# Kernel tuning notes

Hardware: AMD Instinct MI355X
Metric: run time of the kernel (lower is better)

Reference implementation:

```python
import jax, jax.numpy as jnp
import numpy as np

N = 50000
D = 64
E = 800000


def setup_inputs() -> dict:
    key = jax.random.key(0)
    ks = jax.random.split(key, 8)
    x = jax.random.normal(ks[0], (N, D), dtype=jnp.float32)
    edge_index = jax.random.randint(ks[1], (2, E), 0, N, dtype=jnp.int64)
    edge_attr = jax.random.normal(ks[2], (E,), dtype=jnp.float32)
    x_agg_emb = jax.random.normal(ks[3], (N, D), dtype=jnp.float32)
    # Linear(2D -> D) weights stored as [in, out]; scale ~ kaiming-ish
    W_msg = jax.random.normal(ks[4], (2 * D, D), dtype=jnp.float32) * (1.0 / np.sqrt(2 * D))
    b_msg = jnp.zeros((D,), dtype=jnp.float32)
    W_upd = jax.random.normal(ks[5], (2 * D, D), dtype=jnp.float32) * (1.0 / np.sqrt(2 * D))
    b_upd = jnp.zeros((D,), dtype=jnp.float32)
    return {"x": x, "edge_index": edge_index, "edge_attr": edge_attr,
            "x_agg_emb": x_agg_emb, "W_msg": W_msg, "b_msg": b_msg,
            "W_upd": W_upd, "b_upd": b_upd}


def reference(x, edge_index, edge_attr, x_agg_emb, W_msg, b_msg, W_upd, b_upd):
    col, row = edge_index[0], edge_index[1]
    # edge-weighted gather: [E, D]
    msgs = edge_attr[:, None] * x[col]
    # scatter-mean over destination nodes (dim_size = N)
    summed = jax.ops.segment_sum(msgs, row, num_segments=N)            # [N, D]
    counts = jax.ops.segment_sum(jnp.ones_like(edge_attr), row, num_segments=N)  # [N]
    x_agg = summed / jnp.maximum(counts, 1.0)[:, None]
    # message MLP: Linear(2D->D) + ReLU
    m = jax.nn.relu(jnp.concatenate([x_agg, x_agg_emb], axis=-1) @ W_msg + b_msg)
    # update MLP: Linear(2D->D) + ReLU
    out = jax.nn.relu(jnp.concatenate([x, m], axis=-1) @ W_upd + b_upd)
    return out
```

## Files before the change

### kernel.cpp

```cpp
#include <hip/hip_runtime.h>


#define CAP 48
#define FILLB 2048
#define CVTB 1024

typedef __attribute__((ext_vector_type(8))) short short8;
typedef __attribute__((ext_vector_type(4))) float f32x4;

__device__ __forceinline__ unsigned short f2bf(float f) {
    unsigned int u = __float_as_uint(f);
    u += 0x7FFFu + ((u >> 16) & 1u);
    return (unsigned short)(u >> 16);
}
__device__ __forceinline__ float bf2f(unsigned short h) {
    return __uint_as_float((unsigned)h << 16);
}
__device__ __forceinline__ uint4 pack8(const float* v) {
    uint4 r;
    r.x = (unsigned)f2bf(v[0]) | ((unsigned)f2bf(v[1]) << 16);
    r.y = (unsigned)f2bf(v[2]) | ((unsigned)f2bf(v[3]) << 16);
    r.z = (unsigned)f2bf(v[4]) | ((unsigned)f2bf(v[5]) << 16);
    r.w = (unsigned)f2bf(v[6]) | ((unsigned)f2bf(v[7]) << 16);
    return r;
}

__global__ __launch_bounds__(256) void zero_f32(float* p, int n) {
    int i = blockIdx.x * 256 + threadIdx.x;
    if (i < n) p[i] = 0.0f;
}
__global__ __launch_bounds__(256) void zero_i32(int* p, int n) {
    int i = blockIdx.x * 256 + threadIdx.x;
    if (i < n) p[i] = 0;
}

__global__ __launch_bounds__(256) void cvt_zero_group(
    const float* __restrict__ x, unsigned short* __restrict__ xh,
    int* __restrict__ cnt, uint4* __restrict__ pk4, int N)
{
    const int g    = blockIdx.x & 7;
    const int bg   = blockIdx.x >> 3;
    const int nb   = gridDim.x >> 3;
    const int rpg  = (N + 7) >> 3;
    const int rlo  = g * rpg;
    const int rhi  = min(rlo + rpg, N);
    const int nrows = rhi - rlo;
    const int tid  = bg * 256 + (int)threadIdx.x;
    const int nthr = nb * 256;

    for (int c = tid; c < nrows * 8; c += nthr) {
        size_t base = ((size_t)rlo * 8 + c) * 8;
        const float* src = x + base;
        float4 p0 = ((const float4*)src)[0];
        float4 p1 = ((const float4*)src)[1];
        float v[8];
        v[0] = p0.x; v[1] = p0.y; v[2] = p0.z; v[3] = p0.w;
        v[4] = p1.x; v[5] = p1.y; v[6] = p1.z; v[7] = p1.w;
        *(uint4*)&xh[base] = pack8(v);
    }
    for (int c = tid; c < nrows; c += nthr) cnt[rlo + c] = 0;
    const uint4 z = make_uint4(0u, 0u, 0u, 0u);
    const size_t pbase = (size_t)rlo * (CAP / 2);
    for (size_t c = tid; c < (size_t)nrows * (CAP / 2); c += nthr)
        pk4[pbase + c] = z;
}

__global__ __launch_bounds__(256) void fill_group_kernel(
    const int* __restrict__ ei, const float* __restrict__ ea,
    int* cnt, int2* __restrict__ packed, int E, int N)
{
    const int g   = blockIdx.x & 7;
    const int bg  = blockIdx.x >> 3;
    const int nb  = gridDim.x >> 3;
    const int rpg = (N + 7) >> 3;
    const int rlo = g * rpg;
    const int rhi = min(rlo + rpg, N);
    const int chunk = (E + nb - 1) / nb;
    const int lo = bg * chunk;
    const int hi = min(lo + chunk, E);
    int e = lo + (int)threadIdx.x;
    for (; e + 768 < hi; e += 1024) {
        int r0 = ei[E + e];
        int r1 = ei[E + e + 256];
        int r2 = ei[E + e + 512];
        int r3 = ei[E + e + 768];
        int c0 = ei[e], c1 = ei[e + 256], c2 = ei[e + 512], c3 = ei[e + 768];
        float a0 = ea[e], a1 = ea[e + 256], a2 = ea[e + 512], a3 = ea[e + 768];
        bool m0 = (r0 >= rlo) & (r0 < rhi);
        bool m1 = (r1 >= rlo) & (r1 < rhi);
        bool m2 = (r2 >= rlo) & (r2 < rhi);
        bool m3 = (r3 >= rlo) & (r3 < rhi);
        int p0 = CAP, p1 = CAP, p2 = CAP, p3 = CAP;
        if (m0) p0 = atomicAdd(&cnt[r0], 1);
        if (m1) p1 = atomicAdd(&cnt[r1], 1);
        if (m2) p2 = atomicAdd(&cnt[r2], 1);
        if (m3) p3 = atomicAdd(&cnt[r3], 1);
        if (m0 && p0 < CAP) packed[(size_t)r0 * CAP + p0] = make_int2(c0, __float_as_int(a0));
        if (m1 && p1 < CAP) packed[(size_t)r1 * CAP + p1] = make_int2(c1, __float_as_int(a1));
        if (m2 && p2 < CAP) packed[(size_t)r2 * CAP + p2] = make_int2(c2, __float_as_int(a2));
        if (m3 && p3 < CAP) packed[(size_t)r3 * CAP + p3] = make_int2(c3, __float_as_int(a3));
    }
    for (; e < hi; e += 256) {
        int row = ei[E + e];
        if (row >= rlo && row < rhi) {
            int pos = atomicAdd(&cnt[row], 1);
            if (pos < CAP)
                packed[(size_t)row * CAP + pos] = make_int2(ei[e], __float_as_int(ea[e]));
        }
    }
}


__device__ __forceinline__ void stage_W512(
    unsigned short* Wb, const float* Wg, int t)
{
    #pragma unroll
    for (int c = t; c < 1024; c += 512) {
        int R = c >> 6, nn = c & 63;
        int kt = R >> 2, qq = R & 3;
        const float* src = Wg + (size_t)(kt * 32 + qq * 8) * 64 + nn;
        float v[8];
        #pragma unroll
        for (int j = 0; j < 8; j++) v[j] = src[(size_t)j * 64];
        *(uint4*)&Wb[R * 528 + nn * 8] = pack8(v);
    }
}

#define CONSUME(D)                                                          \
    {                                                                       \
        unsigned short u0[8], u1[8];                                        \
        _Pragma("unroll")                                                   \
        for (int n = 0; n < 8; n++) {                                       \
            unsigned v0 = ((unsigned)D[n].x << 7) + lane2;                  \
            unsigned v1 = ((unsigned)D[n].z << 7) + lane2;                  \
            u0[n] = *(const unsigned short*)((const char*)xh + v0);         \
            u1[n] = *(const unsigned short*)((const char*)xh + v1);         \
        }                                                                   \
        _Pragma("unroll")                                                   \
        for (int n = 0; n < 8; n++) {                                       \
            ac0[n] += __int_as_float(D[n].y) * bf2f(u0[n]);                 \
            ac1[n] += __int_as_float(D[n].w) * bf2f(u1[n]);                 \
        }                                                                   \
    }

__global__ __launch_bounds__(512) void gather_mlp(
    const int2* __restrict__ packed, const int* __restrict__ cnt,
    const unsigned short* __restrict__ xh, const float* __restrict__ emb,
    const float* __restrict__ Wm, const float* __restrict__ bm,
    const float* __restrict__ Wu, const float* __restrict__ bu,
    float* __restrict__ out, int N)
{
    __shared__ __align__(16) unsigned short Ab [64 * 128];
    __shared__ __align__(16) unsigned short Ab2[64 * 128];
    __shared__ __align__(16) unsigned short Wb [16 * 528];
    __shared__ __align__(16) unsigned short Wb2[16 * 528];

    const int t    = threadIdx.x;
    const int g    = blockIdx.x & 7;
    const int tile = blockIdx.x >> 3;
    const int rpg  = (N + 7) >> 3;
    const int rlo  = g * rpg;
    const int rhi  = min(rlo + rpg, N);
    const int tile0 = rlo + tile * 64;
    const int lane = t & 63;
    const int q = lane >> 4, ln = lane & 15;
    const unsigned lane2 = (unsigned)lane * 2;
    const int wu = __builtin_amdgcn_readfirstlane(t >> 6);

    stage_W512(Wb,  Wm, t);
    stage_W512(Wb2, Wu, t);
    {
        int r = t >> 3, c = t & 7;
        int node = tile0 + r;
        uint4 d = make_uint4(0u, 0u, 0u, 0u);
        if (node < rhi)
            d = *(const uint4*)&xh[(size_t)node * 64 + c * 8];
        *(uint4*)&Ab2[r * 128 + ((c ^ (r & 15)) * 8)] = d;
    }
    {
        int r = t >> 3, c = t & 7;
        int node = tile0 + r;
        float v[8] = {0.f, 0.f, 0.f, 0.f, 0.f, 0.f, 0.f, 0.f};
        if (node < rhi) {
            const float* src = emb + (size_t)node * 64 + c * 8;
            float4 p0 = ((const float4*)src)[0];
            float4 p1 = ((const float4*)src)[1];
            v[0] = p0.x; v[1] = p0.y; v[2] = p0.z; v[3] = p0.w;
            v[4] = p1.x; v[5] = p1.y; v[6] = p1.z; v[7] = p1.w;
        }
        int ch = 8 + c;
        *(uint4*)&Ab[r * 128 + ((ch ^ (r & 15)) * 8)] = pack8(v);
    }

    const int4* s4 = (const int4*)packed;
    int seg[8], deg[8];
    int maxdl = 0;
    #pragma unroll
    for (int n = 0; n < 8; n++) {
        int node = tile0 + wu * 8 + n;
        bool ok = node < rhi;
        int nd = ok ? node : rlo;
        seg[n] = nd * (CAP / 2);
        deg[n] = ok ? cnt[node] : 0;
        maxdl  = max(maxdl, ok ? min(deg[n], CAP) : 0);
    }
    float ac0[8], ac1[8];
    #pragma unroll
    for (int n = 0; n < 8; n++) { ac0[n] = 0.f; ac1[n] = 0.f; }

    int maxb = (maxdl + 1) >> 1;
    int4 dc[8], dn[8];
    #pragma unroll
    for (int n = 0; n < 8; n++) dc[n] = s4[seg[n]];
    int jb = 0;
    while (jb < maxb) {
        int jn = min(jb + 1, CAP / 2 - 1);
        #pragma unroll
        for (int n = 0; n < 8; n++) dn[n] = s4[seg[n] + jn];
        CONSUME(dc);
        jb++;
        if (jb >= maxb) break;
        int jn2 = min(jb + 1, CAP / 2 - 1);
        #pragma unroll
        for (int n = 0; n < 8; n++) dc[n] = s4[seg[n] + jn2];
        CONSUME(dn);
        jb++;
    }

    #pragma unroll
    for (int n = 0; n < 8; n++) {
        int r = wu * 8 + n;
        int node = tile0 + r;
        float mean = (node < rhi)
            ? (ac0[n] + ac1[n]) / fmaxf((float)deg[n], 1.0f) : 0.f;
        int ch = lane >> 3;
        Ab[r * 128 + ((ch ^ (r & 15)) * 8) + (lane & 7)] = f2bf(mean);
    }
    __syncthreads();

    const int wr = wu & 3;
    const int wn0 = (wu >> 2) * 2, wn1 = wn0 + 1;
    f32x4 acc0 = (f32x4){0.f, 0.f, 0.f, 0.f};
    f32x4 acc1 = (f32x4){0.f, 0.f, 0.f, 0.f};
    {
        const int rr = wr * 16 + ln;
        #pragma unroll
        for (int kt = 0; kt < 4; kt++) {
            short8 af = *(const short8*)&Ab[rr * 128 + (((kt * 4 + q) ^ ln) * 8)];
            short8 bf0 = *(const short8*)&Wb[(kt * 4 + q) * 528 + (wn0 * 16 + ln) * 8];
            short8 bf1 = *(const short8*)&Wb[(kt * 4 + q) * 528 + (wn1 * 16 + ln) * 8];
            acc0 = __builtin_amdgcn_mfma_f32_16x16x32_bf16(af, bf0, acc0, 0, 0, 0);
            acc1 = __builtin_amdgcn_mfma_f32_16x16x32_bf16(af, bf1, acc1, 0, 0, 0);
        }
    }

    {
        float bmv0 = bm[wn0 * 16 + ln];
        float bmv1 = bm[wn1 * 16 + ln];
        #pragma unroll
        for (int reg = 0; reg < 4; reg++) {
            int rr = wr * 16 + q * 4 + reg;
            {
                float mv = fmaxf(acc0[reg] + bmv0, 0.f);
                int k  = 64 + wn0 * 16 + ln;
                int ch = k >> 3;
                Ab2[rr * 128 + ((ch ^ (rr & 15)) * 8) + (k & 7)] = f2bf(mv);
            }
            {
                float mv = fmaxf(acc1[reg] + bmv1, 0.f);
                int k  = 64 + wn1 * 16 + ln;
                int ch = k >> 3;
                Ab2[rr * 128 + ((ch ^ (rr & 15)) * 8) + (k & 7)] = f2bf(mv);
            }
        }
    }
    __syncthreads();

    f32x4 acc2a = (f32x4){0.f, 0.f, 0.f, 0.f};
    f32x4 acc2b = (f32x4){0.f, 0.f, 0.f, 0.f};
    {
        const int rr = wr * 16 + ln;
        #pragma unroll
        for (int kt = 0; kt < 4; kt++) {
            short8 af = *(const short8*)&Ab2[rr * 128 + (((kt * 4 + q) ^ ln) * 8)];
            short8 bf0 = *(const short8*)&Wb2[(kt * 4 + q) * 528 + (wn0 * 16 + ln) * 8];
            short8 bf1 = *(const short8*)&Wb2[(kt * 4 + q) * 528 + (wn1 * 16 + ln) * 8];
            acc2a = __builtin_amdgcn_mfma_f32_16x16x32_bf16(af, bf0, acc2a, 0, 0, 0);
            acc2b = __builtin_amdgcn_mfma_f32_16x16x32_bf16(af, bf1, acc2b, 0, 0, 0);
        }
    }
    {
        float buv0 = bu[wn0 * 16 + ln];
        float buv1 = bu[wn1 * 16 + ln];
        #pragma unroll
        for (int reg = 0; reg < 4; reg++) {
            int rr = wr * 16 + q * 4 + reg;
            int node = tile0 + rr;
            if (node < rhi) {
                out[(size_t)node * 64 + wn0 * 16 + ln] = fmaxf(acc2a[reg] + buv0, 0.f);
                out[(size_t)node * 64 + wn1 * 16 + ln] = fmaxf(acc2b[reg] + buv1, 0.f);
            }
        }
    }
}


__global__ __launch_bounds__(256) void hist_kernel(
    const int* __restrict__ ei, int* hist, int E)
{
    int e = blockIdx.x * 256 + threadIdx.x;
    if (e < E) atomicAdd(&hist[ei[E + e]], 1);
}
__global__ __launch_bounds__(256) void scan_partial_kernel(
    const int* __restrict__ hist, int* partial, int N)
{
    __shared__ int s[256];
    int t = threadIdx.x;
    int i = blockIdx.x * 256 + t;
    s[t] = (i < N) ? hist[i] : 0;
    __syncthreads();
    #pragma unroll
    for (int off = 128; off > 0; off >>= 1) {
        if (t < off) s[t] += s[t + off];
        __syncthreads();
    }
    if (t == 0) partial[blockIdx.x] = s[0];
}
__global__ __launch_bounds__(256) void scan_top_kernel(
    const int* __restrict__ partial, int* scanP, int NB)
{
    __shared__ int s[256];
    int t = threadIdx.x;
    int v = (t < NB) ? partial[t] : 0;
    s[t] = v;
    __syncthreads();
    #pragma unroll
    for (int off = 1; off < 256; off <<= 1) {
        int add = (t >= off) ? s[t - off] : 0;
        __syncthreads();
        s[t] += add;
        __syncthreads();
    }
    if (t < NB) scanP[t] = s[t] - v;
}
__global__ __launch_bounds__(256) void scan_final_kernel(
    const int* __restrict__ hist, const int* __restrict__ scanP,
    int* offsets, int* cursor, int N)
{
    __shared__ int s[256];
    int t = threadIdx.x;
    int i = blockIdx.x * 256 + t;
    int v = (i < N) ? hist[i] : 0;
    s[t] = v;
    __syncthreads();
    #pragma unroll
    for (int off = 1; off < 256; off <<= 1) {
        int add = (t >= off) ? s[t - off] : 0;
        __syncthreads();
        s[t] += add;
        __syncthreads();
    }
    if (i < N) {
        int o = scanP[blockIdx.x] + s[t] - v;
        offsets[i] = o;
        cursor[i]  = o;
    }
}
__global__ __launch_bounds__(256) void fill_kernel(
    const int* __restrict__ ei, const float* __restrict__ ea,
    int* cursor, int2* __restrict__ packed, int E)
{
    int e = blockIdx.x * 256 + threadIdx.x;
    if (e >= E) return;
    int pos = atomicAdd(&cursor[ei[E + e]], 1);
    packed[pos] = make_int2(ei[e], __float_as_int(ea[e]));
}
__global__ __launch_bounds__(256) void gather_kernel(
    const int2* __restrict__ packed, const int* __restrict__ offsets,
    const int* __restrict__ hist, const float* __restrict__ x,
    float* __restrict__ out, int N)
{
    int t = threadIdx.x;
    int n = blockIdx.x * 4 + (t >> 6);
    int lane = t & 63;
    if (n >= N) return;
    int start = offsets[n];
    int deg   = hist[n];
    float a0 = 0.f, a1 = 0.f, a2 = 0.f, a3 = 0.f;
    int j = 0;
    for (; j + 4 <= deg; j += 4) {
        int2 p0 = packed[start + j];
        int2 p1 = packed[start + j + 1];
        int2 p2 = packed[start + j + 2];
        int2 p3 = packed[start + j + 3];
        a0 += __int_as_float(p0.y) * x[(size_t)p0.x * 64 + lane];
        a1 += __int_as_float(p1.y) * x[(size_t)p1.x * 64 + lane];
        a2 += __int_as_float(p2.y) * x[(size_t)p2.x * 64 + lane];
        a3 += __int_as_float(p3.y) * x[(size_t)p3.x * 64 + lane];
    }
    for (; j < deg; j++) {
        int2 p = packed[start + j];
        a0 += __int_as_float(p.y) * x[(size_t)p.x * 64 + lane];
    }
    float acc = (a0 + a1) + (a2 + a3);
    out[(size_t)n * 64 + lane] = acc / fmaxf((float)deg, 1.0f);
}


__global__ __launch_bounds__(256) void scatter_kernel(
    const int* __restrict__ ei, const float* __restrict__ ea,
    const float* __restrict__ x, float* summed, float* counts, int E)
{
    int idx = blockIdx.x * 256 + threadIdx.x;
    int e = idx >> 6;
    int d = idx & 63;
    if (e >= E) return;
    float v = ea[e] * x[(size_t)ei[e] * 64 + d];
    atomicAdd(&summed[(size_t)ei[E + e] * 64 + d], v);
    if (d == 0) atomicAdd(&counts[ei[E + e]], 1.0f);
}


__device__ __forceinline__ void stage_W(
    unsigned short* Wb, const float* Wg, int t)
{
    #pragma unroll
    for (int c = t; c < 1024; c += 256) {
        int R = c >> 6, nn = c & 63;
        int kt = R >> 2, qq = R & 3;
        const float* src = Wg + (size_t)(kt * 32 + qq * 8) * 64 + nn;
        float v[8];
        #pragma unroll
        for (int j = 0; j < 8; j++) v[j] = src[(size_t)j * 64];
        *(uint4*)&Wb[R * 528 + nn * 8] = pack8(v);
    }
}

__device__ __forceinline__ void mfma_tile(
    const unsigned short* Ab, const unsigned short* Wb,
    int wv, int lane, f32x4 acc[4])
{
    const int q  = lane >> 4;
    const int ln = lane & 15;
    const int rr = wv * 16 + ln;
    short8 af[4];
    #pragma unroll
    for (int kt = 0; kt < 4; kt++)
        af[kt] = *(const short8*)&Ab[rr * 128 + (((kt * 4 + q) ^ ln) * 8)];
    #pragma unroll
    for (int nt = 0; nt < 4; nt++) {
        #pragma unroll
        for (int kt = 0; kt < 4; kt++) {
            short8 bf = *(const short8*)&Wb[(kt * 4 + q) * 528 + (nt * 16 + ln) * 8];
            acc[nt] = __builtin_amdgcn_mfma_f32_16x16x32_bf16(af[kt], bf, acc[nt], 0, 0, 0);
        }
    }
}

__global__ __launch_bounds__(256) void mfma_mlp(
    const float* Aagg, const float* __restrict__ Aemb,
    const float* __restrict__ counts, const float* __restrict__ Xin,
    const float* __restrict__ Wm, const float* __restrict__ bm,
    const float* __restrict__ Wu, const float* __restrict__ bu,
    float* out, int N)
{
    __shared__ __align__(16) unsigned short Ab[64 * 128];
    __shared__ __align__(16) unsigned short Wb[16 * 528];

    const int t = threadIdx.x;
    const int tile0 = blockIdx.x * 64;
    const int lane = t & 63, wv = t >> 6;
    const int q = lane >> 4, ln = lane & 15;

    stage_W(Wb, Wm, t);
    #pragma unroll
    for (int s = t; s < 1024; s += 256) {
        int r = s >> 4, chunk = s & 15;
        int node = tile0 + r;
        float v[8] = {0.f, 0.f, 0.f, 0.f, 0.f, 0.f, 0.f, 0.f};
        if (node < N) {
            const float* src = (chunk < 8)
                ? (Aagg + (size_t)node * 64 + chunk * 8)
                : (Aemb + (size_t)node * 64 + (chunk - 8) * 8);
            float4 p0 = ((const float4*)src)[0];
            float4 p1 = ((const float4*)src)[1];
            v[0] = p0.x; v[1] = p0.y; v[2] = p0.z; v[3] = p0.w;
            v[4] = p1.x; v[5] = p1.y; v[6] = p1.z; v[7] = p1.w;
            if (counts && chunk < 8) {
                float rc = 1.0f / fmaxf(counts[node], 1.0f);
                #pragma unroll
                for (int i = 0; i < 8; i++) v[i] *= rc;
            }
        }
        *(uint4*)&Ab[r * 128 + ((chunk ^ (r & 15)) * 8)] = pack8(v);
    }
    __syncthreads();

    f32x4 acc[4];
    #pragma unroll
    for (int nt = 0; nt < 4; nt++) acc[nt] = (f32x4){0.f, 0.f, 0.f, 0.f};
    mfma_tile(Ab, Wb, wv, lane, acc);
    __syncthreads();

    stage_W(Wb, Wu, t);
    #pragma unroll
    for (int s = t; s < 512; s += 256) {
        int r = s >> 3, chunk = s & 7;
        int node = tile0 + r;
        float v[8] = {0.f, 0.f, 0.f, 0.f, 0.f, 0.f, 0.f, 0.f};
        if (node < N) {
            const float* src = Xin + (size_t)node * 64 + chunk * 8;
            float4 p0 = ((const float4*)src)[0];
            float4 p1 = ((const float4*)src)[1];
            v[0] = p0.x; v[1] = p0.y; v[2] = p0.z; v[3] = p0.w;
            v[4] = p1.x; v[5] = p1.y; v[6] = p1.z; v[7] = p1.w;
        }
        *(uint4*)&Ab[r * 128 + ((chunk ^ (r & 15)) * 8)] = pack8(v);
    }
    #pragma unroll
    for (int nt = 0; nt < 4; nt++) {
        float bmv = bm[nt * 16 + ln];
        #pragma unroll
        for (int reg = 0; reg < 4; reg++) {
            float mv = fmaxf(acc[nt][reg] + bmv, 0.f);
            int rr = wv * 16 + q * 4 + reg;
            int k  = 64 + nt * 16 + ln;
            int ch = k >> 3;
            Ab[rr * 128 + ((ch ^ (rr & 15)) * 8) + (k & 7)] = f2bf(mv);
        }
    }
    __syncthreads();

    f32x4 acc2[4];
    #pragma unroll
    for (int nt = 0; nt < 4; nt++) acc2[nt] = (f32x4){0.f, 0.f, 0.f, 0.f};
    mfma_tile(Ab, Wb, wv, lane, acc2);
    #pragma unroll
    for (int nt = 0; nt < 4; nt++) {
        float buv = bu[nt * 16 + ln];
        #pragma unroll
        for (int reg = 0; reg < 4; reg++) {
            int rr = wv * 16 + q * 4 + reg;
            int node = tile0 + rr;
            if (node < N)
                out[(size_t)node * 64 + nt * 16 + ln] =
                    fmaxf(acc2[nt][reg] + buv, 0.f);
        }
    }
}

extern "C" void kernel_launch(void* const* d_in, const int* in_sizes, int n_in,
                              void* d_out, int out_size, void* d_ws, size_t ws_size,
                              hipStream_t stream) {
    const float* x   = (const float*)d_in[0];
    const int*   ei  = (const int*)d_in[1];
    const float* ea  = (const float*)d_in[2];
    const float* emb = (const float*)d_in[3];
    const float* Wm  = (const float*)d_in[4];
    const float* bm  = (const float*)d_in[5];
    const float* Wu  = (const float*)d_in[6];
    const float* bu  = (const float*)d_in[7];
    float*       out = (float*)d_out;

    const int N = in_sizes[0] / 64;
    const int E = in_sizes[2];
    const int NB = (N + 255) / 256;

    const int eblocks = (E + 255) / 256;
    const int mblocks = (N + 63) / 64;
    const int rpg = (N + 7) / 8;

    const size_t need_cap = (size_t)N * CAP * 8 + (size_t)N * 128 + (size_t)N * 4;
    const size_t need_csr = (size_t)E * 8 + ((size_t)3 * N + 512) * 4;

    if (ws_size >= need_cap) {
        char* ws = (char*)d_ws;
        int2*           packed = (int2*)ws;
        unsigned short* xh     = (unsigned short*)(ws + (size_t)N * CAP * 8);
        int*            cnt    = (int*)(ws + (size_t)N * CAP * 8 + (size_t)N * 128);

        cvt_zero_group<<<CVTB, 256, 0, stream>>>(x, xh, cnt, (uint4*)packed, N);
        fill_group_kernel<<<FILLB, 256, 0, stream>>>(ei, ea, cnt, packed, E, N);
        int tpg = (rpg + 63) / 64;
        gather_mlp<<<8 * tpg, 512, 0, stream>>>(packed, cnt, xh, emb,
                                                Wm, bm, Wu, bu, out, N);
    } else if (ws_size >= need_csr && NB <= 256) {
        char* ws = (char*)d_ws;
        int2* packed  = (int2*)ws;
        int*  hist    = (int*)(ws + (size_t)E * 8);
        int*  offsets = hist + N;
        int*  cursor  = offsets + N;
        int*  partial = cursor + N;
        int*  scanP   = partial + 256;

        zero_i32<<<NB, 256, 0, stream>>>(hist, N);
        hist_kernel<<<eblocks, 256, 0, stream>>>(ei, hist, E);
        scan_partial_kernel<<<NB, 256, 0, stream>>>(hist, partial, N);
        scan_top_kernel<<<1, 256, 0, stream>>>(partial, scanP, NB);
        scan_final_kernel<<<NB, 256, 0, stream>>>(hist, scanP, offsets, cursor, N);
        fill_kernel<<<eblocks, 256, 0, stream>>>(ei, ea, cursor, packed, E);
        gather_kernel<<<(N + 3) / 4, 256, 0, stream>>>(packed, offsets, hist, x, out, N);
        mfma_mlp<<<mblocks, 256, 0, stream>>>(out, emb, nullptr, x,
                                              Wm, bm, Wu, bu, out, N);
    } else {
        float* counts = (float*)d_ws;
        zero_f32<<<(N * 64 + 255) / 256, 256, 0, stream>>>(out, N * 64);
        zero_f32<<<NB, 256, 0, stream>>>(counts, N);
        long long total = (long long)E * 64;
        scatter_kernel<<<(int)((total + 255) / 256), 256, 0, stream>>>(
            ei, ea, x, out, counts, E);
        mfma_mlp<<<mblocks, 256, 0, stream>>>(out, emb, counts, x,
                                              Wm, bm, Wu, bu, out, N);
    }
}
```

Before: 163.5 us.

## Reuse one LDS activation buffer and simplify gather loop for higher occupancy

Drops the second 16 KB activation buffer by holding the x tile in registers and writing it into the same buffer after the first MLP, with an extra barrier. The gather loop loses its explicit double-buffered prefetch of edge records and now loads per-iteration in two groups of four nodes. Degree is made wave-uniform and a min-waves launch bound is added. Together these cut LDS and register use to fit more blocks per CU, at the cost of less explicit memory-latency hiding within each wave.

```diff
diff --git a/kernel.cpp b/kernel.cpp
--- a/kernel.cpp
+++ b/kernel.cpp
@@ -126,24 +126,7 @@
     }
 }
 
-#define CONSUME(D)                                                          \
-    {                                                                       \
-        unsigned short u0[8], u1[8];                                        \
-        _Pragma("unroll")                                                   \
-        for (int n = 0; n < 8; n++) {                                       \
-            unsigned v0 = ((unsigned)D[n].x << 7) + lane2;                  \
-            unsigned v1 = ((unsigned)D[n].z << 7) + lane2;                  \
-            u0[n] = *(const unsigned short*)((const char*)xh + v0);         \
-            u1[n] = *(const unsigned short*)((const char*)xh + v1);         \
-        }                                                                   \
-        _Pragma("unroll")                                                   \
-        for (int n = 0; n < 8; n++) {                                       \
-            ac0[n] += __int_as_float(D[n].y) * bf2f(u0[n]);                 \
-            ac1[n] += __int_as_float(D[n].w) * bf2f(u1[n]);                 \
-        }                                                                   \
-    }
-
-__global__ __launch_bounds__(512) void gather_mlp(
+__global__ __launch_bounds__(512, 6) void gather_mlp(
     const int2* __restrict__ packed, const int* __restrict__ cnt,
     const unsigned short* __restrict__ xh, const float* __restrict__ emb,
     const float* __restrict__ Wm, const float* __restrict__ bm,
@@ -151,7 +134,6 @@
     float* __restrict__ out, int N)
 {
     __shared__ __align__(16) unsigned short Ab [64 * 128];
-    __shared__ __align__(16) unsigned short Ab2[64 * 128];
     __shared__ __align__(16) unsigned short Wb [16 * 528];
     __shared__ __align__(16) unsigned short Wb2[16 * 528];
 
@@ -169,62 +151,80 @@
 
     stage_W512(Wb,  Wm, t);
     stage_W512(Wb2, Wu, t);
+    const int sr = t >> 3, sc = t & 7;
+    uint4 xreg = make_uint4(0u, 0u, 0u, 0u);
+    if (tile0 + sr < rhi)
+        xreg = *(const uint4*)&xh[(size_t)(tile0 + sr) * 64 + sc * 8];
     {
-        int r = t >> 3, c = t & 7;
-        int node = tile0 + r;
-        uint4 d = make_uint4(0u, 0u, 0u, 0u);
-        if (node < rhi)
-            d = *(const uint4*)&xh[(size_t)node * 64 + c * 8];
-        *(uint4*)&Ab2[r * 128 + ((c ^ (r & 15)) * 8)] = d;
-    }
-    {
-        int r = t >> 3, c = t & 7;
-        int node = tile0 + r;
+        int node = tile0 + sr;
         float v[8] = {0.f, 0.f, 0.f, 0.f, 0.f, 0.f, 0.f, 0.f};
         if (node < rhi) {
-            const float* src = emb + (size_t)node * 64 + c * 8;
+            const float* src = emb + (size_t)node * 64 + sc * 8;
             float4 p0 = ((const float4*)src)[0];
             float4 p1 = ((const float4*)src)[1];
             v[0] = p0.x; v[1] = p0.y; v[2] = p0.z; v[3] = p0.w;
             v[4] = p1.x; v[5] = p1.y; v[6] = p1.z; v[7] = p1.w;
         }
-        int ch = 8 + c;
-        *(uint4*)&Ab[r * 128 + ((ch ^ (r & 15)) * 8)] = pack8(v);
-    }
-
-    const int4* s4 = (const int4*)packed;
-    int seg[8], deg[8];
+        int ch = 8 + sc;
+        *(uint4*)&Ab[sr * 128 + ((ch ^ (sr & 15)) * 8)] = pack8(v);
+    }
+
+    const int4* sp[8];
+    int deg[8];
     int maxdl = 0;
     #pragma unroll
     for (int n = 0; n < 8; n++) {
         int node = tile0 + wu * 8 + n;
         bool ok = node < rhi;
         int nd = ok ? node : rlo;
-        seg[n] = nd * (CAP / 2);
-        deg[n] = ok ? cnt[node] : 0;
-        maxdl  = max(maxdl, ok ? min(deg[n], CAP) : 0);
+        sp[n] = (const int4*)packed + (size_t)nd * (CAP / 2);
+        deg[n] = ok ? __builtin_amdgcn_readfirstlane(cnt[node]) : 0;
+        maxdl = max(maxdl, min(deg[n], CAP));
     }
     float ac0[8], ac1[8];
     #pragma unroll
     for (int n = 0; n < 8; n++) { ac0[n] = 0.f; ac1[n] = 0.f; }
 
-    int maxb = (maxdl + 1) >> 1;
-    int4 dc[8], dn[8];
-    #pragma unroll
-    for (int n = 0; n < 8; n++) dc[n] = s4[seg[n]];
-    int jb = 0;
-    while (jb < maxb) {
-        int jn = min(jb + 1, CAP / 2 - 1);
-        #pragma unroll
-        for (int n = 0; n < 8; n++) dn[n] = s4[seg[n] + jn];
-        CONSUME(dc);
-        jb++;
-        if (jb >= maxb) break;
-        int jn2 = min(jb + 1, CAP / 2 - 1);
-        #pragma unroll
-        for (int n = 0; n < 8; n++) dc[n] = s4[seg[n] + jn2];
-        CONSUME(dn);
-        jb++;
+    const int maxb = (maxdl + 1) >> 1;
+    for (int jb = 0; jb < maxb; jb++) {
+        {
+            int4 d0 = sp[0][jb], d1 = sp[1][jb], d2 = sp[2][jb], d3 = sp[3][jb];
+            unsigned short u00 = *(const unsigned short*)((const char*)xh + (((unsigned)d0.x << 7) + lane2));
+            unsigned short u01 = *(const unsigned short*)((const char*)xh + (((unsigned)d0.z << 7) + lane2));
+            unsigned short u10 = *(const unsigned short*)((const char*)xh + (((unsigned)d1.x << 7) + lane2));
+            unsigned short u11 = *(const unsigned short*)((const char*)xh + (((unsigned)d1.z << 7) + lane2));
+            unsigned short u20 = *(const unsigned short*)((const char*)xh + (((unsigned)d2.x << 7) + lane2));
+            unsigned short u21 = *(const unsigned short*)((const char*)xh + (((unsigned)d2.z << 7) + lane2));
+            unsigned short u30 = *(const unsigned short*)((const char*)xh + (((unsigned)d3.x << 7) + lane2));
+            unsigned short u31 = *(const unsigned short*)((const char*)xh + (((unsigned)d3.z << 7) + lane2));
+            ac0[0] += __int_as_float(d0.y) * bf2f(u00);
+            ac1[0] += __int_as_float(d0.w) * bf2f(u01);
+            ac0[1] += __int_as_float(d1.y) * bf2f(u10);
+            ac1[1] += __int_as_float(d1.w) * bf2f(u11);
+            ac0[2] += __int_as_float(d2.y) * bf2f(u20);
+            ac1[2] += __int_as_float(d2.w) * bf2f(u21);
+            ac0[3] += __int_as_float(d3.y) * bf2f(u30);
+            ac1[3] += __int_as_float(d3.w) * bf2f(u31);
+        }
+        {
+            int4 d0 = sp[4][jb], d1 = sp[5][jb], d2 = sp[6][jb], d3 = sp[7][jb];
+            unsigned short u00 = *(const unsigned short*)((const char*)xh + (((unsigned)d0.x << 7) + lane2));
+            unsigned short u01 = *(const unsigned short*)((const char*)xh + (((unsigned)d0.z << 7) + lane2));
+            unsigned short u10 = *(const unsigned short*)((const char*)xh + (((unsigned)d1.x << 7) + lane2));
+            unsigned short u11 = *(const unsigned short*)((const char*)xh + (((unsigned)d1.z << 7) + lane2));
+            unsigned short u20 = *(const unsigned short*)((const char*)xh + (((unsigned)d2.x << 7) + lane2));
+            unsigned short u21 = *(const unsigned short*)((const char*)xh + (((unsigned)d2.z << 7) + lane2));
+            unsigned short u30 = *(const unsigned short*)((const char*)xh + (((unsigned)d3.x << 7) + lane2));
+            unsigned short u31 = *(const unsigned short*)((const char*)xh + (((unsigned)d3.z << 7) + lane2));
+            ac0[4] += __int_as_float(d0.y) * bf2f(u00);
+            ac1[4] += __int_as_float(d0.w) * bf2f(u01);
+            ac0[5] += __int_as_float(d1.y) * bf2f(u10);
+            ac1[5] += __int_as_float(d1.w) * bf2f(u11);
+            ac0[6] += __int_as_float(d2.y) * bf2f(u20);
+            ac1[6] += __int_as_float(d2.w) * bf2f(u21);
+            ac0[7] += __int_as_float(d3.y) * bf2f(u30);
+            ac1[7] += __int_as_float(d3.w) * bf2f(u31);
+        }
     }
 
     #pragma unroll
@@ -253,7 +253,9 @@
             acc1 = __builtin_amdgcn_mfma_f32_16x16x32_bf16(af, bf1, acc1, 0, 0, 0);
         }
     }
-
+    __syncthreads();
+
+    *(uint4*)&Ab[sr * 128 + ((sc ^ (sr & 15)) * 8)] = xreg;
     {
         float bmv0 = bm[wn0 * 16 + ln];
         float bmv1 = bm[wn1 * 16 + ln];
@@ -264,13 +266,13 @@
                 float mv = fmaxf(acc0[reg] + bmv0, 0.f);
                 int k  = 64 + wn0 * 16 + ln;
                 int ch = k >> 3;
-                Ab2[rr * 128 + ((ch ^ (rr & 15)) * 8) + (k & 7)] = f2bf(mv);
+                Ab[rr * 128 + ((ch ^ (rr & 15)) * 8) + (k & 7)] = f2bf(mv);
             }
             {
                 float mv = fmaxf(acc1[reg] + bmv1, 0.f);
                 int k  = 64 + wn1 * 16 + ln;
                 int ch = k >> 3;
-                Ab2[rr * 128 + ((ch ^ (rr & 15)) * 8) + (k & 7)] = f2bf(mv);
+                Ab[rr * 128 + ((ch ^ (rr & 15)) * 8) + (k & 7)] = f2bf(mv);
             }
         }
     }
@@ -282,7 +284,7 @@
         const int rr = wr * 16 + ln;
         #pragma unroll
         for (int kt = 0; kt < 4; kt++) {
-            short8 af = *(const short8*)&Ab2[rr * 128 + (((kt * 4 + q) ^ ln) * 8)];
+            short8 af = *(const short8*)&Ab[rr * 128 + (((kt * 4 + q) ^ ln) * 8)];
             short8 bf0 = *(const short8*)&Wb2[(kt * 4 + q) * 528 + (wn0 * 16 + ln) * 8];
             short8 bf1 = *(const short8*)&Wb2[(kt * 4 + q) * 528 + (wn1 * 16 + ln) * 8];
             acc2a = __builtin_amdgcn_mfma_f32_16x16x32_bf16(af, bf0, acc2a, 0, 0, 0);
```

Result: no change. 163.8 us (+0.2%).
